# Kernel optimization log

Measured on AMD Instinct MI355X. Metric: run time of the kernel, lower is better.

Reference implementation:

```python
import jax, jax.numpy as jnp
import numpy as np

H = 2048          # hidden_size
I = 768           # moe_intermediate_size
E = 64            # num_experts
TOP_K = 8         # num_experts_per_tok (norm_topk_prob=True)
B, S = 1, 1024


def setup_inputs() -> dict:
    key = jax.random.key(0)
    ks = jax.random.split(key, 5)
    scale = 0.02
    return {
        "hidden_states": jax.random.normal(ks[0], (B, S, H), dtype=jnp.float32),
        "W_router": jax.random.normal(ks[1], (H, E), dtype=jnp.float32) * scale,
        "W_gate": jax.random.normal(ks[2], (E, H, I), dtype=jnp.float32) * scale,
        "W_up": jax.random.normal(ks[3], (E, H, I), dtype=jnp.float32) * scale,
        "W_down": jax.random.normal(ks[4], (E, I, H), dtype=jnp.float32) * scale,
    }


def reference(hidden_states, W_router, W_gate, W_up, W_down):
    b, s, h = hidden_states.shape
    x = hidden_states.reshape(-1, h)                      # [T, H]

    # --- Qwen3MoeTopKRouter: linear gate -> fp32 softmax -> top-k -> renorm ---
    logits = x @ W_router                                 # [T, E]
    probs = jax.nn.softmax(logits.astype(jnp.float32), axis=-1)
    top_w, top_idx = jax.lax.top_k(probs, TOP_K)          # [T, K]
    top_w = top_w / jnp.sum(top_w, axis=-1, keepdims=True)  # norm_topk_prob
    top_w = top_w.astype(x.dtype)

    # combine weights per (token, expert): zero if expert not selected
    comb = jnp.sum(jax.nn.one_hot(top_idx, E, dtype=x.dtype) * top_w[..., None], axis=1)  # [T, E]

    # --- per-expert SwiGLU MLP: down(silu(gate(x)) * up(x)), dense-masked ---
    g = jnp.einsum('th,ehi->eti', x, W_gate)              # [E, T, I]
    u = jnp.einsum('th,ehi->eti', x, W_up)                # [E, T, I]
    hmid = jax.nn.silu(g) * u                             # [E, T, I]
    # fold combine weight into the intermediate to avoid an [E, T, H] buffer
    hmid = hmid * comb.T[:, :, None]                      # [E, T, I]
    out = jnp.einsum('eti,eih->th', hmid, W_down)         # [T, H]

    return out.reshape(b, s, h)
```

## Files before the change

kernel.cpp:

```cpp
#include <hip/hip_runtime.h>
#include <hip/hip_bf16.h>

#define H_DIM 2048
#define I_DIM 768
#define NEXP 64
#define TOPK 8
#define NTOK 1024
#define BM 256
#define BKS 32

typedef float f32x4 __attribute__((ext_vector_type(4)));
typedef unsigned int u32x4 __attribute__((ext_vector_type(4)));
typedef unsigned int u32x2 __attribute__((ext_vector_type(2)));
typedef short bf16v8 __attribute__((ext_vector_type(8)));
typedef unsigned short u16x8 __attribute__((ext_vector_type(8)));
typedef unsigned int u32;

#define NTLOAD __builtin_nontemporal_load

#define WS_NEEDED 50954752ull

__device__ inline unsigned short f2bf(float f) {
    union { float f; u32 u; } v; v.f = f;
    u32 r = (v.u + 0x7FFFu + ((v.u >> 16) & 1u)) >> 16;
    return (unsigned short)r;
}
__device__ inline u32 pack2(float a, float b) {
    return (u32)f2bf(a) | ((u32)f2bf(b) << 16);
}

__device__ inline void async16(void* l, const void* g) {
    __builtin_amdgcn_global_load_lds(
        (const __attribute__((address_space(1))) unsigned int*)g,
        (__attribute__((address_space(3))) unsigned int*)l, 16, 0, 0);
}

__global__ void zero_kernel(float4* p, int n4) {
    int i = blockIdx.x * blockDim.x + threadIdx.x;
    if (i < n4) p[i] = (float4){0.f, 0.f, 0.f, 0.f};
}

__global__ __launch_bounds__(512) void router_kernel(
    const float* __restrict__ x, const float* __restrict__ Wr,
    int* __restrict__ topk_idx, float* __restrict__ topk_w,
    ushort4* __restrict__ xbf)
{
    const int t   = blockIdx.x;
    const int tid = threadIdx.x;
    const int lane = tid & 63;
    const int wv   = tid >> 6;
    __shared__ float xs[H_DIM];
    __shared__ float red[8][64];

    const float* xrow = x + (size_t)t * H_DIM;
    {
        const float4* src = (const float4*)xrow;
        float4 v = src[tid];
        ((float4*)xs)[tid] = v;
        ushort4 o;
        o.x = f2bf(v.x); o.y = f2bf(v.y); o.z = f2bf(v.z); o.w = f2bf(v.w);
        xbf[(size_t)t * (H_DIM / 4) + tid] = o;
    }
    __syncthreads();

    float acc = 0.f;
    const int h0 = wv * 256;
    #pragma unroll 8
    for (int h = h0; h < h0 + 256; ++h) acc += xs[h] * Wr[(size_t)h * NEXP + lane];
    red[wv][lane] = acc;
    __syncthreads();

    if (tid < 64) {
        const int e = tid;
        float logit = ((red[0][e] + red[1][e]) + (red[2][e] + red[3][e]))
                    + ((red[4][e] + red[5][e]) + (red[6][e] + red[7][e]));

        float m = logit;
        #pragma unroll
        for (int o = 32; o > 0; o >>= 1) m = fmaxf(m, __shfl_xor(m, o));
        float p = __expf(logit - m);
        float s = p;
        #pragma unroll
        for (int o = 32; o > 0; o >>= 1) s += __shfl_xor(s, o);
        float prob = p / s;

        float myp = prob;
        float kw[TOPK]; int kid[TOPK]; float wsum = 0.f;
        #pragma unroll
        for (int k = 0; k < TOPK; ++k) {
            float v = myp; int bi = e;
            #pragma unroll
            for (int o = 32; o > 0; o >>= 1) {
                float ov = __shfl_xor(v, o);
                int   oi = __shfl_xor(bi, o);
                if (ov > v || (ov == v && oi < bi)) { v = ov; bi = oi; }
            }
            kw[k] = v; kid[k] = bi; wsum += v;
            if (e == bi) myp = -1.f;
        }
        if (e == 0) {
            float inv = 1.f / wsum;
            #pragma unroll
            for (int k = 0; k < TOPK; ++k) {
                topk_idx[t * TOPK + k] = kid[k];
                topk_w[t * TOPK + k]   = kw[k] * inv;
            }
        }
    }
}

__global__ __launch_bounds__(64) void listbuild_kernel(
    const int* __restrict__ topk_idx, const float* __restrict__ topk_w,
    int* __restrict__ counts, int* __restrict__ lists, float* __restrict__ wlist,
    int* __restrict__ invmap)
{
    const int e = blockIdx.x;
    const int lane = threadIdx.x;
    int n = 0;
    for (int base = 0; base < NTOK * TOPK; base += 64) {
        int s = base + lane;
        int idx = topk_idx[s];
        bool match = (idx == e);
        unsigned long long mask = __ballot(match);
        int pre = __popcll(mask & ((1ull << lane) - 1ull));
        if (match) {
            lists[e * NTOK + n + pre] = s >> 3;
            wlist[e * NTOK + n + pre] = topk_w[s];
            invmap[s] = n + pre;
        }
        n += __popcll(mask);
    }
    if (lane == 0) counts[e] = n;
}

__global__ __launch_bounds__(64) void scan_kernel(
    const int* __restrict__ counts, int* __restrict__ offsets)
{
    int e = threadIdx.x;
    int v = counts[e];
    int xacc = v;
    #pragma unroll
    for (int o = 1; o < 64; o <<= 1) {
        int y = __shfl_up(xacc, o);
        if (e >= o) xacc += y;
    }
    offsets[e] = xacc - v;
}

#define MFMA_BF16 __builtin_amdgcn_mfma_f32_16x16x32_bf16
#define LGKM0()  asm volatile("s_waitcnt lgkmcnt(0)" ::: "memory")
#define RAWBAR() __builtin_amdgcn_s_barrier()
#define VMCNT4() asm volatile("s_waitcnt vmcnt(4)" ::: "memory")
#define VMCNT0() asm volatile("s_waitcnt vmcnt(0)" ::: "memory")
#define FENCE()  asm volatile("" ::: "memory")

__global__ __launch_bounds__(512) void gateup_kernel(
    const unsigned short* __restrict__ xbf,
    const float* __restrict__ Wg, const float* __restrict__ Wu,
    const int* __restrict__ counts, const int* __restrict__ offsets,
    const int* __restrict__ lists, const float* __restrict__ wlist,
    unsigned short* __restrict__ hmid)
{
    const int b  = blockIdx.x;
    const int wg = (b & 7) * 192 + (b >> 3);
    const int itile = wg % 24;
    const int e     = wg / 24;

    const int count = counts[e];
    if (count == 0) return;
    const int off = offsets[e];
    const int i0 = itile * 32;

    __shared__ unsigned short Alds[2][BM][32];
    __shared__ u32 Bgl[2][32 * 20];
    __shared__ u32 Bul[2][32 * 20];

    const int tid  = threadIdx.x;
    const int lane = tid & 63;
    const int wid  = tid >> 6;
    const int wm   = wid >> 1, wn = wid & 1;
    const int kb   = lane >> 4;
    const int l15  = lane & 15;

    const int bnn  = tid & 31;
    const int bkq  = (tid >> 5) & 7;
    const int bmat = tid >> 8;
    const float* WB = (bmat ? Wu : Wg) + (size_t)e * H_DIM * I_DIM + i0 + bnn;
    const int key4w = 4 * ((bnn >> 3) & 3);
    const int bwoff = bnn * 20 + ((2 * bkq) ^ key4w);
    const int brn   = wn * 16 + l15;
    const int key4r = 4 * ((brn >> 3) & 3);

    const int c4  = lane & 3;
    const int r0  = wid * 32 + (lane >> 2);
    const int r1  = r0 + 16;
    const int awr0 = wid * 32;
    const int awr1 = wid * 32 + 16;
    const int aoff = (wm * 64 + l15) * 32 + ((kb ^ ((l15 >> 1) & 3)) * 8);

    for (int mstart = 0; mstart < count; mstart += BM) {
        int p0 = mstart + r0; if (p0 >= count) p0 = count - 1;
        int p1 = mstart + r1; if (p1 >= count) p1 = count - 1;
        const unsigned short* srcA0 = xbf + (size_t)lists[e * NTOK + p0] * H_DIM
                                      + (size_t)((c4 ^ ((r0 >> 1) & 3)) * 8);
        const unsigned short* srcA1 = xbf + (size_t)lists[e * NTOK + p1] * H_DIM
                                      + (size_t)((c4 ^ ((r1 >> 1) & 3)) * 8);
        const bool mact = (mstart + wm * 64) < count;

        f32x4 accg[4], accu[4];
        #pragma unroll
        for (int i = 0; i < 4; ++i) {
            accg[i] = (f32x4){0.f, 0.f, 0.f, 0.f};
            accu[i] = (f32x4){0.f, 0.f, 0.f, 0.f};
        }

        float bA0, bA1, bA2, bA3;
        float bB0, bB1, bB2, bB3;

#define GU_LOADB(R0,R1,R2,R3,h)                                                 \
        {                                                                       \
            R0 = NTLOAD(WB + (size_t)((h) + 4 * bkq)     * I_DIM);              \
            R1 = NTLOAD(WB + (size_t)((h) + 4 * bkq + 1) * I_DIM);              \
            R2 = NTLOAD(WB + (size_t)((h) + 4 * bkq + 2) * I_DIM);              \
            R3 = NTLOAD(WB + (size_t)((h) + 4 * bkq + 3) * I_DIM);              \
        }
#define GU_STOREB(BUF,R0,R1,R2,R3)                                              \
        {                                                                       \
            u32x2 w_; w_.x = pack2(R0, R1); w_.y = pack2(R2, R3);               \
            *(u32x2*)((bmat ? Bul[BUF] : Bgl[BUF]) + bwoff) = w_;               \
        }
#define GU_DMAA(BUF,h)                                                          \
        {                                                                       \
            async16((void*)&Alds[BUF][awr0][0], (const void*)(srcA0 + (h)));    \
            async16((void*)&Alds[BUF][awr1][0], (const void*)(srcA1 + (h)));    \
        }
#define GU_MFMA(BUF)                                                            \
        if (mact) {                                                             \
            const unsigned short* Ab_ = (const unsigned short*)Alds[BUF];       \
            bf16v8 af[4], bg, bu;                                               \
            _Pragma("unroll")                                                   \
            for (int mf = 0; mf < 4; ++mf)                                      \
                af[mf] = *(const bf16v8*)&Ab_[aoff + mf * 512];                 \
            bg = *(const bf16v8*)&Bgl[BUF][brn * 20 + ((4 * kb) ^ key4r)];      \
            bu = *(const bf16v8*)&Bul[BUF][brn * 20 + ((4 * kb) ^ key4r)];      \
            _Pragma("unroll")                                                   \
            for (int mf = 0; mf < 4; ++mf) {                                    \
                accg[mf] = MFMA_BF16(af[mf], bg, accg[mf], 0, 0, 0);            \
                accu[mf] = MFMA_BF16(af[mf], bu, accu[mf], 0, 0, 0);            \
            }                                                                   \
        }
#define GU_PHASE(BUF,OBUF,R0,R1,R2,R3,nhB,nhA,VM)                               \
        GU_STOREB(BUF, R0, R1, R2, R3);                                         \
        if ((nhB) < H_DIM) GU_LOADB(R0, R1, R2, R3, (nhB));                     \
        VM();                                                                   \
        LGKM0();                                                                \
        RAWBAR();                                                               \
        FENCE();                                                                \
        if ((nhA) < H_DIM) GU_DMAA(OBUF, (nhA));                                \
        FENCE();                                                                \
        __builtin_amdgcn_s_setprio(1);                                          \
        GU_MFMA(BUF);                                                           \
        __builtin_amdgcn_s_setprio(0);

        GU_LOADB(bA0, bA1, bA2, bA3, 0);
        GU_LOADB(bB0, bB1, bB2, bB3, BKS);
        GU_DMAA(0, 0);

        for (int hh = 0; hh < H_DIM - 2 * BKS; hh += 2 * BKS) {
            GU_PHASE(0, 1, bA0, bA1, bA2, bA3, hh + 2 * BKS, hh + BKS,     VMCNT4);
            GU_PHASE(1, 0, bB0, bB1, bB2, bB3, hh + 3 * BKS, hh + 2 * BKS, VMCNT4);
        }
        GU_PHASE(0, 1, bA0, bA1, bA2, bA3, H_DIM, H_DIM - BKS, VMCNT0);
        GU_PHASE(1, 0, bB0, bB1, bB2, bB3, H_DIM, H_DIM,       VMCNT0);
        __syncthreads();
#undef GU_LOADB
#undef GU_STOREB
#undef GU_DMAA
#undef GU_MFMA
#undef GU_PHASE

        if (mact) {
            #pragma unroll
            for (int mf = 0; mf < 4; ++mf)
                #pragma unroll
                for (int r = 0; r < 4; ++r) {
                    int pos = mstart + wm * 64 + mf * 16 + kb * 4 + r;
                    if (pos < count) {
                        float wgt = wlist[e * NTOK + pos];
                        float g = accg[mf][r], u = accu[mf][r];
                        float s = 1.f / (1.f + __expf(-g));
                        hmid[(size_t)(off + pos) * I_DIM + i0 + wn * 16 + l15] = f2bf(g * s * u * wgt);
                    }
                }
        }
    }
}

template <bool USE_PART>
__global__ __launch_bounds__(512) void down_kernel(
    const unsigned short* __restrict__ hmid, const float* __restrict__ Wd,
    const int* __restrict__ counts, const int* __restrict__ offsets,
    const int* __restrict__ lists, float* __restrict__ out,
    unsigned short* __restrict__ part)
{
    const int b  = blockIdx.x;
    const int wg = (b & 7) * 512 + (b >> 3);
    const int htile = wg % 64;
    const int e     = wg / 64;

    const int count = counts[e];
    if (count == 0) return;
    const int off = offsets[e];
    const int h0 = htile * 32;

    __shared__ unsigned short Alds[2][BM][32];
    __shared__ u32 Bdl[2][32 * 20];

    const int tid  = threadIdx.x;
    const int lane = tid & 63;
    const int wid  = tid >> 6;
    const int wm   = wid >> 1, wn = wid & 1;
    const int kb   = lane >> 4;
    const int l15  = lane & 15;

    const int bnn  = tid & 31;
    const int bkq  = (tid >> 5) & 7;
    const bool bact = tid < 256;
    const float* WB = Wd + (size_t)e * I_DIM * H_DIM + h0 + bnn;
    const int key4w = 4 * ((bnn >> 3) & 3);
    const int bwoff = bnn * 20 + ((2 * bkq) ^ key4w);
    const int brn   = wn * 16 + l15;
    const int key4r = 4 * ((brn >> 3) & 3);

    const int c4  = lane & 3;
    const int r0  = wid * 32 + (lane >> 2);
    const int r1  = r0 + 16;
    const int awr0 = wid * 32;
    const int awr1 = wid * 32 + 16;
    const int aoff = (wm * 64 + l15) * 32 + ((kb ^ ((l15 >> 1) & 3)) * 8);

    for (int mstart = 0; mstart < count; mstart += BM) {
        int p0 = mstart + r0; if (p0 >= count) p0 = count - 1;
        int p1 = mstart + r1; if (p1 >= count) p1 = count - 1;
        const unsigned short* srcA0 = hmid + (size_t)(off + p0) * I_DIM
                                      + (size_t)((c4 ^ ((r0 >> 1) & 3)) * 8);
        const unsigned short* srcA1 = hmid + (size_t)(off + p1) * I_DIM
                                      + (size_t)((c4 ^ ((r1 >> 1) & 3)) * 8);
        const bool mact = (mstart + wm * 64) < count;

        f32x4 acc[4];
        #pragma unroll
        for (int i = 0; i < 4; ++i) acc[i] = (f32x4){0.f, 0.f, 0.f, 0.f};

        float bA0, bA1, bA2, bA3;
        float bB0, bB1, bB2, bB3;

#define DN_LOADB(R0,R1,R2,R3,k)                                                 \
        if (bact) {                                                             \
            R0 = NTLOAD(WB + (size_t)((k) + 4 * bkq)     * H_DIM);              \
            R1 = NTLOAD(WB + (size_t)((k) + 4 * bkq + 1) * H_DIM);              \
            R2 = NTLOAD(WB + (size_t)((k) + 4 * bkq + 2) * H_DIM);              \
            R3 = NTLOAD(WB + (size_t)((k) + 4 * bkq + 3) * H_DIM);              \
        }
#define DN_STOREB(BUF,R0,R1,R2,R3)                                              \
        if (bact) {                                                             \
            u32x2 w_; w_.x = pack2(R0, R1); w_.y = pack2(R2, R3);               \
            *(u32x2*)(Bdl[BUF] + bwoff) = w_;                                   \
        }
#define DN_DMAA(BUF,k)                                                          \
        {                                                                       \
            async16((void*)&Alds[BUF][awr0][0], (const void*)(srcA0 + (k)));    \
            async16((void*)&Alds[BUF][awr1][0], (const void*)(srcA1 + (k)));    \
        }
#define DN_MFMA(BUF)                                                            \
        if (mact) {                                                             \
            const unsigned short* Ab_ = (const unsigned short*)Alds[BUF];       \
            bf16v8 af[4], bd;                                                   \
            _Pragma("unroll")                                                   \
            for (int mf = 0; mf < 4; ++mf)                                      \
                af[mf] = *(const bf16v8*)&Ab_[aoff + mf * 512];                 \
            bd = *(const bf16v8*)&Bdl[BUF][brn * 20 + ((4 * kb) ^ key4r)];      \
            _Pragma("unroll")                                                   \
            for (int mf = 0; mf < 4; ++mf)                                      \
                acc[mf] = MFMA_BF16(af[mf], bd, acc[mf], 0, 0, 0);              \
        }
#define DN_VMS()  { if (bact) { VMCNT4(); } else { VMCNT0(); } }
#define DN_VMT()  VMCNT0()
#define DN_PHASE(BUF,OBUF,R0,R1,R2,R3,nkB,nkA,VM)                               \
        DN_STOREB(BUF, R0, R1, R2, R3);                                         \
        if ((nkB) < I_DIM) DN_LOADB(R0, R1, R2, R3, (nkB));                     \
        VM();                                                                   \
        LGKM0();                                                                \
        RAWBAR();                                                               \
        FENCE();                                                                \
        if ((nkA) < I_DIM) DN_DMAA(OBUF, (nkA));                                \
        FENCE();                                                                \
        __builtin_amdgcn_s_setprio(1);                                          \
        DN_MFMA(BUF);                                                           \
        __builtin_amdgcn_s_setprio(0);

        DN_LOADB(bA0, bA1, bA2, bA3, 0);
        DN_LOADB(bB0, bB1, bB2, bB3, BKS);
        DN_DMAA(0, 0);

        for (int ii = 0; ii < I_DIM - 2 * BKS; ii += 2 * BKS) {
            DN_PHASE(0, 1, bA0, bA1, bA2, bA3, ii + 2 * BKS, ii + BKS,     DN_VMS);
            DN_PHASE(1, 0, bB0, bB1, bB2, bB3, ii + 3 * BKS, ii + 2 * BKS, DN_VMS);
        }
        DN_PHASE(0, 1, bA0, bA1, bA2, bA3, I_DIM, I_DIM - BKS, DN_VMT);
        DN_PHASE(1, 0, bB0, bB1, bB2, bB3, I_DIM, I_DIM,       DN_VMT);
        __syncthreads();
#undef DN_LOADB
#undef DN_STOREB
#undef DN_DMAA
#undef DN_MFMA
#undef DN_VMS
#undef DN_VMT
#undef DN_PHASE

        if (mact) {
            #pragma unroll
            for (int mf = 0; mf < 4; ++mf)
                #pragma unroll
                for (int r = 0; r < 4; ++r) {
                    int pos = mstart + wm * 64 + mf * 16 + kb * 4 + r;
                    if (pos < count) {
                        if constexpr (USE_PART) {
                            part[(size_t)(off + pos) * H_DIM + h0 + wn * 16 + l15] =
                                f2bf(acc[mf][r]);
                        } else {
                            int tok = lists[e * NTOK + pos];
                            atomicAdd(&out[(size_t)tok * H_DIM + h0 + wn * 16 + l15],
                                      acc[mf][r]);
                        }
                    }
                }
        }
    }
}

__global__ __launch_bounds__(256) void reduce_kernel(
    const unsigned short* __restrict__ part,
    const int* __restrict__ topk_idx, const int* __restrict__ invmap,
    const int* __restrict__ offsets, float* __restrict__ out)
{
    const int t   = blockIdx.x;
    const int tid = threadIdx.x;
    __shared__ int slots[TOPK];
    if (tid < TOPK) {
        int s = t * TOPK + tid;
        slots[tid] = offsets[topk_idx[s]] + invmap[s];
    }
    __syncthreads();

    const int c = tid * 8;
    float acc[8] = {0.f, 0.f, 0.f, 0.f, 0.f, 0.f, 0.f, 0.f};
    #pragma unroll
    for (int k = 0; k < TOPK; ++k) {
        u16x8 v = *(const u16x8*)&part[(size_t)slots[k] * H_DIM + c];
        #pragma unroll
        for (int j = 0; j < 8; ++j)
            acc[j] += __uint_as_float((u32)(unsigned short)v[j] << 16);
    }
    float4* dst = (float4*)&out[(size_t)t * H_DIM + c];
    dst[0] = (float4){acc[0], acc[1], acc[2], acc[3]};
    dst[1] = (float4){acc[4], acc[5], acc[6], acc[7]};
}

extern "C" void kernel_launch(void* const* d_in, const int* in_sizes, int n_in,
                              void* d_out, int out_size, void* d_ws, size_t ws_size,
                              hipStream_t stream) {
    const float* x  = (const float*)d_in[0];
    const float* Wr = (const float*)d_in[1];
    const float* Wg = (const float*)d_in[2];
    const float* Wu = (const float*)d_in[3];
    const float* Wd = (const float*)d_in[4];
    float* out = (float*)d_out;

    char* ws = (char*)d_ws;
    int*   topk_idx = (int*)  (ws + 0);
    float* topk_w   = (float*)(ws + 32768);
    int*   counts   = (int*)  (ws + 65536);
    int*   offsets  = (int*)  (ws + 65792);
    int*   lists    = (int*)  (ws + 66048);
    float* wlist    = (float*)(ws + 328192);
    int*   invmap   = (int*)  (ws + 590336);
    unsigned short* hmid = (unsigned short*)(ws + 623104);
    unsigned short* xbf  = (unsigned short*)(ws + 13206016);
    unsigned short* part = (unsigned short*)(ws + 17400320);

    const bool usePart = ws_size >= WS_NEEDED;

    hipLaunchKernelGGL(router_kernel, dim3(NTOK), dim3(512), 0, stream,
                       x, Wr, topk_idx, topk_w, (ushort4*)xbf);
    hipLaunchKernelGGL(listbuild_kernel, dim3(NEXP), dim3(64), 0, stream,
                       topk_idx, topk_w, counts, lists, wlist, invmap);
    hipLaunchKernelGGL(scan_kernel, dim3(1), dim3(64), 0, stream,
                       counts, offsets);
    hipLaunchKernelGGL(gateup_kernel, dim3(24 * NEXP), dim3(512), 0, stream,
                       xbf, Wg, Wu, counts, offsets, lists, wlist, hmid);
    if (usePart) {
        hipLaunchKernelGGL((down_kernel<true>), dim3(64 * NEXP), dim3(512), 0, stream,
                           hmid, Wd, counts, offsets, lists, out, part);
        hipLaunchKernelGGL(reduce_kernel, dim3(NTOK), dim3(256), 0, stream,
                           part, topk_idx, invmap, offsets, out);
    } else {
        const int nout4 = NTOK * H_DIM / 4;
        hipLaunchKernelGGL(zero_kernel, dim3((nout4 + 255) / 256), dim3(256), 0, stream,
                           (float4*)out, nout4);
        hipLaunchKernelGGL((down_kernel<false>), dim3(64 * NEXP), dim3(512), 0, stream,
                           hmid, Wd, counts, offsets, lists, out, part);
    }
}
```

Before: 479.2 us.

## Widen N tile to 64 columns in gate/up and down expert GEMMs

```diff
diff --git a/kernel.cpp b/kernel.cpp
--- a/kernel.cpp
+++ b/kernel.cpp
@@ -148,11 +148,11 @@
 }
 
 #define MFMA_BF16 __builtin_amdgcn_mfma_f32_16x16x32_bf16
-#define LGKM0()  asm volatile("s_waitcnt lgkmcnt(0)" ::: "memory")
-#define RAWBAR() __builtin_amdgcn_s_barrier()
-#define VMCNT4() asm volatile("s_waitcnt vmcnt(4)" ::: "memory")
-#define VMCNT0() asm volatile("s_waitcnt vmcnt(0)" ::: "memory")
-#define FENCE()  asm volatile("" ::: "memory")
+#define LGKM0()   asm volatile("s_waitcnt lgkmcnt(0)" ::: "memory")
+#define RAWBAR()  __builtin_amdgcn_s_barrier()
+#define VMCNT8()  asm volatile("s_waitcnt vmcnt(8)" ::: "memory")
+#define VMCNT0()  asm volatile("s_waitcnt vmcnt(0)" ::: "memory")
+#define FENCE()   asm volatile("" ::: "memory")
 
 __global__ __launch_bounds__(512) void gateup_kernel(
     const unsigned short* __restrict__ xbf,
@@ -162,18 +162,18 @@
     unsigned short* __restrict__ hmid)
 {
     const int b  = blockIdx.x;
-    const int wg = (b & 7) * 192 + (b >> 3);
-    const int itile = wg % 24;
-    const int e     = wg / 24;
+    const int wg = (b & 7) * 96 + (b >> 3);
+    const int itile = wg % 12;
+    const int e     = wg / 12;
 
     const int count = counts[e];
     if (count == 0) return;
     const int off = offsets[e];
-    const int i0 = itile * 32;
+    const int i0 = itile * 64;
 
     __shared__ unsigned short Alds[2][BM][32];
-    __shared__ u32 Bgl[2][32 * 20];
-    __shared__ u32 Bul[2][32 * 20];
+    __shared__ u32 Bgl[2][64 * 20];
+    __shared__ u32 Bul[2][64 * 20];
 
     const int tid  = threadIdx.x;
     const int lane = tid & 63;
@@ -182,14 +182,16 @@
     const int kb   = lane >> 4;
     const int l15  = lane & 15;
 
-    const int bnn  = tid & 31;
-    const int bkq  = (tid >> 5) & 7;
+    const int bnn  = tid & 63;
+    const int bkq  = (tid >> 6) & 3;
     const int bmat = tid >> 8;
     const float* WB = (bmat ? Wu : Wg) + (size_t)e * H_DIM * I_DIM + i0 + bnn;
     const int key4w = 4 * ((bnn >> 3) & 3);
-    const int bwoff = bnn * 20 + ((2 * bkq) ^ key4w);
-    const int brn   = wn * 16 + l15;
-    const int key4r = 4 * ((brn >> 3) & 3);
+    const int bwoff = bnn * 20 + ((4 * bkq) ^ key4w);
+    const int brn0 = wn * 32 + l15;
+    const int brn1 = wn * 32 + 16 + l15;
+    const int key0 = 4 * ((brn0 >> 3) & 3);
+    const int key1 = 4 * ((brn1 >> 3) & 3);
 
     const int c4  = lane & 3;
     const int r0  = wid * 32 + (lane >> 2);
@@ -207,27 +209,32 @@
                                       + (size_t)((c4 ^ ((r1 >> 1) & 3)) * 8);
         const bool mact = (mstart + wm * 64) < count;
 
-        f32x4 accg[4], accu[4];
+        f32x4 accg[4][2], accu[4][2];
         #pragma unroll
-        for (int i = 0; i < 4; ++i) {
-            accg[i] = (f32x4){0.f, 0.f, 0.f, 0.f};
-            accu[i] = (f32x4){0.f, 0.f, 0.f, 0.f};
-        }
-
-        float bA0, bA1, bA2, bA3;
-        float bB0, bB1, bB2, bB3;
-
-#define GU_LOADB(R0,R1,R2,R3,h)                                                 \
+        for (int i = 0; i < 4; ++i)
+            #pragma unroll
+            for (int j = 0; j < 2; ++j) {
+                accg[i][j] = (f32x4){0.f, 0.f, 0.f, 0.f};
+                accu[i][j] = (f32x4){0.f, 0.f, 0.f, 0.f};
+            }
+
+        float sA0, sA1, sA2, sA3, sA4, sA5, sA6, sA7;
+        float sB0, sB1, sB2, sB3, sB4, sB5, sB6, sB7;
+
+#define GU_LOADB(S0,S1,S2,S3,S4,S5,S6,S7,h)                                     \
         {                                                                       \
-            R0 = NTLOAD(WB + (size_t)((h) + 4 * bkq)     * I_DIM);              \
-            R1 = NTLOAD(WB + (size_t)((h) + 4 * bkq + 1) * I_DIM);              \
-            R2 = NTLOAD(WB + (size_t)((h) + 4 * bkq + 2) * I_DIM);              \
-            R3 = NTLOAD(WB + (size_t)((h) + 4 * bkq + 3) * I_DIM);              \
-        }
-#define GU_STOREB(BUF,R0,R1,R2,R3)                                              \
+            const float* p_ = WB + (size_t)((h) + 8 * bkq) * I_DIM;             \
+            S0 = NTLOAD(p_);             S1 = NTLOAD(p_ + I_DIM);               \
+            S2 = NTLOAD(p_ + 2 * I_DIM); S3 = NTLOAD(p_ + 3 * I_DIM);           \
+            S4 = NTLOAD(p_ + 4 * I_DIM); S5 = NTLOAD(p_ + 5 * I_DIM);           \
+            S6 = NTLOAD(p_ + 6 * I_DIM); S7 = NTLOAD(p_ + 7 * I_DIM);           \
+        }
+#define GU_STOREB(BUF,S0,S1,S2,S3,S4,S5,S6,S7)                                  \
         {                                                                       \
-            u32x2 w_; w_.x = pack2(R0, R1); w_.y = pack2(R2, R3);               \
-            *(u32x2*)((bmat ? Bul[BUF] : Bgl[BUF]) + bwoff) = w_;               \
+            u32x4 w_;                                                           \
+            w_.x = pack2(S0, S1); w_.y = pack2(S2, S3);                         \
+            w_.z = pack2(S4, S5); w_.w = pack2(S6, S7);                         \
+            *(u32x4*)((bmat ? Bul[BUF] : Bgl[BUF]) + bwoff) = w_;               \
         }
 #define GU_DMAA(BUF,h)                                                          \
         {                                                                       \
@@ -237,41 +244,50 @@
 #define GU_MFMA(BUF)                                                            \
         if (mact) {                                                             \
             const unsigned short* Ab_ = (const unsigned short*)Alds[BUF];       \
-            bf16v8 af[4], bg, bu;                                               \
+            bf16v8 af[4];                                                       \
             _Pragma("unroll")                                                   \
             for (int mf = 0; mf < 4; ++mf)                                      \
                 af[mf] = *(const bf16v8*)&Ab_[aoff + mf * 512];                 \
-            bg = *(const bf16v8*)&Bgl[BUF][brn * 20 + ((4 * kb) ^ key4r)];      \
-            bu = *(const bf16v8*)&Bul[BUF][brn * 20 + ((4 * kb) ^ key4r)];      \
+            bf16v8 bg0 = *(const bf16v8*)&Bgl[BUF][brn0 * 20 + ((4 * kb) ^ key0)]; \
+            bf16v8 bg1 = *(const bf16v8*)&Bgl[BUF][brn1 * 20 + ((4 * kb) ^ key1)]; \
+            bf16v8 bu0 = *(const bf16v8*)&Bul[BUF][brn0 * 20 + ((4 * kb) ^ key0)]; \
+            bf16v8 bu1 = *(const bf16v8*)&Bul[BUF][brn1 * 20 + ((4 * kb) ^ key1)]; \
             _Pragma("unroll")                                                   \
             for (int mf = 0; mf < 4; ++mf) {                                    \
-                accg[mf] = MFMA_BF16(af[mf], bg, accg[mf], 0, 0, 0);            \
-                accu[mf] = MFMA_BF16(af[mf], bu, accu[mf], 0, 0, 0);            \
+                accg[mf][0] = MFMA_BF16(af[mf], bg0, accg[mf][0], 0, 0, 0);     \
+                accg[mf][1] = MFMA_BF16(af[mf], bg1, accg[mf][1], 0, 0, 0);     \
+                accu[mf][0] = MFMA_BF16(af[mf], bu0, accu[mf][0], 0, 0, 0);     \
+                accu[mf][1] = MFMA_BF16(af[mf], bu1, accu[mf][1], 0, 0, 0);     \
             }                                                                   \
         }
-#define GU_PHASE(BUF,OBUF,R0,R1,R2,R3,nhB,nhA,VM)                               \
-        GU_STOREB(BUF, R0, R1, R2, R3);                                         \
-        if ((nhB) < H_DIM) GU_LOADB(R0, R1, R2, R3, (nhB));                     \
+#define GU_PHASE(PB,S0,S1,S2,S3,S4,S5,S6,S7,nhB,nhA,VM)                         \
+        GU_STOREB(PB, S0, S1, S2, S3, S4, S5, S6, S7);                          \
+        if ((nhB) < H_DIM) GU_LOADB(S0, S1, S2, S3, S4, S5, S6, S7, (nhB));     \
         VM();                                                                   \
         LGKM0();                                                                \
         RAWBAR();                                                               \
         FENCE();                                                                \
-        if ((nhA) < H_DIM) GU_DMAA(OBUF, (nhA));                                \
+        if ((nhA) < H_DIM) GU_DMAA(PB ^ 1, (nhA));                              \
         FENCE();                                                                \
         __builtin_amdgcn_s_setprio(1);                                          \
-        GU_MFMA(BUF);                                                           \
+        GU_MFMA(PB);                                                            \
         __builtin_amdgcn_s_setprio(0);
 
-        GU_LOADB(bA0, bA1, bA2, bA3, 0);
-        GU_LOADB(bB0, bB1, bB2, bB3, BKS);
         GU_DMAA(0, 0);
-
-        for (int hh = 0; hh < H_DIM - 2 * BKS; hh += 2 * BKS) {
-            GU_PHASE(0, 1, bA0, bA1, bA2, bA3, hh + 2 * BKS, hh + BKS,     VMCNT4);
-            GU_PHASE(1, 0, bB0, bB1, bB2, bB3, hh + 3 * BKS, hh + 2 * BKS, VMCNT4);
-        }
-        GU_PHASE(0, 1, bA0, bA1, bA2, bA3, H_DIM, H_DIM - BKS, VMCNT0);
-        GU_PHASE(1, 0, bB0, bB1, bB2, bB3, H_DIM, H_DIM,       VMCNT0);
+        GU_LOADB(sA0, sA1, sA2, sA3, sA4, sA5, sA6, sA7, 0);
+        GU_LOADB(sB0, sB1, sB2, sB3, sB4, sB5, sB6, sB7, BKS);
+
+        for (int t2 = 0; t2 < 31; ++t2) {
+            const int hh = t2 * 2 * BKS;
+            GU_PHASE(0, sA0, sA1, sA2, sA3, sA4, sA5, sA6, sA7,
+                     hh + 2 * BKS, hh + BKS,     VMCNT8);
+            GU_PHASE(1, sB0, sB1, sB2, sB3, sB4, sB5, sB6, sB7,
+                     hh + 3 * BKS, hh + 2 * BKS, VMCNT8);
+        }
+        GU_PHASE(0, sA0, sA1, sA2, sA3, sA4, sA5, sA6, sA7,
+                 H_DIM, 63 * BKS, VMCNT0);
+        GU_PHASE(1, sB0, sB1, sB2, sB3, sB4, sB5, sB6, sB7,
+                 H_DIM, H_DIM,    VMCNT0);
         __syncthreads();
 #undef GU_LOADB
 #undef GU_STOREB
@@ -283,15 +299,18 @@
             #pragma unroll
             for (int mf = 0; mf < 4; ++mf)
                 #pragma unroll
-                for (int r = 0; r < 4; ++r) {
-                    int pos = mstart + wm * 64 + mf * 16 + kb * 4 + r;
-                    if (pos < count) {
-                        float wgt = wlist[e * NTOK + pos];
-                        float g = accg[mf][r], u = accu[mf][r];
-                        float s = 1.f / (1.f + __expf(-g));
-                        hmid[(size_t)(off + pos) * I_DIM + i0 + wn * 16 + l15] = f2bf(g * s * u * wgt);
+                for (int nf = 0; nf < 2; ++nf)
+                    #pragma unroll
+                    for (int r = 0; r < 4; ++r) {
+                        int pos = mstart + wm * 64 + mf * 16 + kb * 4 + r;
+                        if (pos < count) {
+                            float wgt = wlist[e * NTOK + pos];
+                            float g = accg[mf][nf][r], u = accu[mf][nf][r];
+                            float s = 1.f / (1.f + __expf(-g));
+                            hmid[(size_t)(off + pos) * I_DIM + i0 + wn * 32 + nf * 16 + l15]
+                                = f2bf(g * s * u * wgt);
+                        }
                     }
-                }
         }
     }
 }
@@ -304,17 +323,17 @@
     unsigned short* __restrict__ part)
 {
     const int b  = blockIdx.x;
-    const int wg = (b & 7) * 512 + (b >> 3);
-    const int htile = wg % 64;
-    const int e     = wg / 64;
+    const int wg = (b & 7) * 256 + (b >> 3);
+    const int htile = wg % 32;
+    const int e     = wg / 32;
 
     const int count = counts[e];
     if (count == 0) return;
     const int off = offsets[e];
-    const int h0 = htile * 32;
+    const int h0 = htile * 64;
 
     __shared__ unsigned short Alds[2][BM][32];
-    __shared__ u32 Bdl[2][32 * 20];
+    __shared__ u32 Bdl[2][64 * 20];
 
     const int tid  = threadIdx.x;
     const int lane = tid & 63;
@@ -323,14 +342,16 @@
     const int kb   = lane >> 4;
     const int l15  = lane & 15;
 
-    const int bnn  = tid & 31;
-    const int bkq  = (tid >> 5) & 7;
+    const int bnn  = tid & 63;
+    const int bkq  = (tid >> 6) & 3;
     const bool bact = tid < 256;
     const float* WB = Wd + (size_t)e * I_DIM * H_DIM + h0 + bnn;
     const int key4w = 4 * ((bnn >> 3) & 3);
-    const int bwoff = bnn * 20 + ((2 * bkq) ^ key4w);
-    const int brn   = wn * 16 + l15;
-    const int key4r = 4 * ((brn >> 3) & 3);
+    const int bwoff = bnn * 20 + ((4 * bkq) ^ key4w);
+    const int brn0 = wn * 32 + l15;
+    const int brn1 = wn * 32 + 16 + l15;
+    const int key0 = 4 * ((brn0 >> 3) & 3);
+    const int key1 = 4 * ((brn1 >> 3) & 3);
 
     const int c4  = lane & 3;
     const int r0  = wid * 32 + (lane >> 2);
@@ -348,24 +369,29 @@
                                       + (size_t)((c4 ^ ((r1 >> 1) & 3)) * 8);
         const bool mact = (mstart + wm * 64) < count;
 
-        f32x4 acc[4];
+        f32x4 acc[4][2];
         #pragma unroll
-        for (int i = 0; i < 4; ++i) acc[i] = (f32x4){0.f, 0.f, 0.f, 0.f};
-
-        float bA0, bA1, bA2, bA3;
-        float bB0, bB1, bB2, bB3;
-
-#define DN_LOADB(R0,R1,R2,R3,k)                                                 \
+        for (int i = 0; i < 4; ++i)
+            #pragma unroll
+            for (int j = 0; j < 2; ++j) acc[i][j] = (f32x4){0.f, 0.f, 0.f, 0.f};
+
+        float sA0, sA1, sA2, sA3, sA4, sA5, sA6, sA7;
+        float sB0, sB1, sB2, sB3, sB4, sB5, sB6, sB7;
+
+#define DN_LOADB(S0,S1,S2,S3,S4,S5,S6,S7,k)                                     \
         if (bact) {                                                             \
-            R0 = NTLOAD(WB + (size_t)((k) + 4 * bkq)     * H_DIM);              \
-            R1 = NTLOAD(WB + (size_t)((k) + 4 * bkq + 1) * H_DIM);              \
-            R2 = NTLOAD(WB + (size_t)((k) + 4 * bkq + 2) * H_DIM);              \
-            R3 = NTLOAD(WB + (size_t)((k) + 4 * bkq + 3) * H_DIM);              \
-        }
-#define DN_STOREB(BUF,R0,R1,R2,R3)                                              \
+            const float* p_ = WB + (size_t)((k) + 8 * bkq) * H_DIM;             \
+            S0 = NTLOAD(p_);             S1 = NTLOAD(p_ + H_DIM);               \
+            S2 = NTLOAD(p_ + 2 * H_DIM); S3 = NTLOAD(p_ + 3 * H_DIM);           \
+            S4 = NTLOAD(p_ + 4 * H_DIM); S5 = NTLOAD(p_ + 5 * H_DIM);           \
+            S6 = NTLOAD(p_ + 6 * H_DIM); S7 = NTLOAD(p_ + 7 * H_DIM);           \
+        }
+#define DN_STOREB(BUF,S0,S1,S2,S3,S4,S5,S6,S7)                                  \
         if (bact) {                                                             \
-            u32x2 w_; w_.x = pack2(R0, R1); w_.y = pack2(R2, R3);               \
-            *(u32x2*)(Bdl[BUF] + bwoff) = w_;                                   \
+            u32x4 w_;                                                           \
+            w_.x = pack2(S0, S1); w_.y = pack2(S2, S3);                         \
+            w_.z = pack2(S4, S5); w_.w = pack2(S6, S7);                         \
+            *(u32x4*)(Bdl[BUF] + bwoff) = w_;                                   \
         }
 #define DN_DMAA(BUF,k)                                                          \
         {                                                                       \
@@ -375,66 +401,74 @@
 #define DN_MFMA(BUF)                                                            \
         if (mact) {                                                             \
             const unsigned short* Ab_ = (const unsigned short*)Alds[BUF];       \
-            bf16v8 af[4], bd;                                                   \
+            bf16v8 af[4];                                                       \
             _Pragma("unroll")                                                   \
             for (int mf = 0; mf < 4; ++mf)                                      \
                 af[mf] = *(const bf16v8*)&Ab_[aoff + mf * 512];                 \
-            bd = *(const bf16v8*)&Bdl[BUF][brn * 20 + ((4 * kb) ^ key4r)];      \
+            bf16v8 bd0 = *(const bf16v8*)&Bdl[BUF][brn0 * 20 + ((4 * kb) ^ key0)]; \
+            bf16v8 bd1 = *(const bf16v8*)&Bdl[BUF][brn1 * 20 + ((4 * kb) ^ key1)]; \
             _Pragma("unroll")                                                   \
-            for (int mf = 0; mf < 4; ++mf)                                      \
-                acc[mf] = MFMA_BF16(af[mf], bd, acc[mf], 0, 0, 0);              \
-        }
-#define DN_VMS()  { if (bact) { VMCNT4(); } else { VMCNT0(); } }
-#define DN_VMT()  VMCNT0()
-#define DN_PHASE(BUF,OBUF,R0,R1,R2,R3,nkB,nkA,VM)                               \
-        DN_STOREB(BUF, R0, R1, R2, R3);                                         \
-        if ((nkB) < I_DIM) DN_LOADB(R0, R1, R2, R3, (nkB));                     \
+            for (int mf = 0; mf < 4; ++mf) {                                    \
+                acc[mf][0] = MFMA_BF16(af[mf], bd0, acc[mf][0], 0, 0, 0);       \
+                acc[mf][1] = MFMA_BF16(af[mf], bd1, acc[mf][1], 0, 0, 0);       \
+            }                                                                   \
+        }
+#define DN_VMS()  { if (bact) { VMCNT8(); } else { VMCNT0(); } }
+#define DN_PHASE(PB,S0,S1,S2,S3,S4,S5,S6,S7,nkB,nkA,VM)                         \
+        DN_STOREB(PB, S0, S1, S2, S3, S4, S5, S6, S7);                          \
+        if ((nkB) < I_DIM) DN_LOADB(S0, S1, S2, S3, S4, S5, S6, S7, (nkB));     \
         VM();                                                                   \
         LGKM0();                                                                \
         RAWBAR();                                                               \
         FENCE();                                                                \
-        if ((nkA) < I_DIM) DN_DMAA(OBUF, (nkA));                                \
+        if ((nkA) < I_DIM) DN_DMAA(PB ^ 1, (nkA));                              \
         FENCE();                                                                \
         __builtin_amdgcn_s_setprio(1);                                          \
-        DN_MFMA(BUF);                                                           \
+        DN_MFMA(PB);                                                            \
         __builtin_amdgcn_s_setprio(0);
 
-        DN_LOADB(bA0, bA1, bA2, bA3, 0);
-        DN_LOADB(bB0, bB1, bB2, bB3, BKS);
         DN_DMAA(0, 0);
-
-        for (int ii = 0; ii < I_DIM - 2 * BKS; ii += 2 * BKS) {
-            DN_PHASE(0, 1, bA0, bA1, bA2, bA3, ii + 2 * BKS, ii + BKS,     DN_VMS);
-            DN_PHASE(1, 0, bB0, bB1, bB2, bB3, ii + 3 * BKS, ii + 2 * BKS, DN_VMS);
-        }
-        DN_PHASE(0, 1, bA0, bA1, bA2, bA3, I_DIM, I_DIM - BKS, DN_VMT);
-        DN_PHASE(1, 0, bB0, bB1, bB2, bB3, I_DIM, I_DIM,       DN_VMT);
+        DN_LOADB(sA0, sA1, sA2, sA3, sA4, sA5, sA6, sA7, 0);
+        DN_LOADB(sB0, sB1, sB2, sB3, sB4, sB5, sB6, sB7, BKS);
+
+        for (int t2 = 0; t2 < 11; ++t2) {
+            const int ii = t2 * 2 * BKS;
+            DN_PHASE(0, sA0, sA1, sA2, sA3, sA4, sA5, sA6, sA7,
+                     ii + 2 * BKS, ii + BKS,     DN_VMS);
+            DN_PHASE(1, sB0, sB1, sB2, sB3, sB4, sB5, sB6, sB7,
+                     ii + 3 * BKS, ii + 2 * BKS, DN_VMS);
+        }
+        DN_PHASE(0, sA0, sA1, sA2, sA3, sA4, sA5, sA6, sA7,
+                 I_DIM, 23 * BKS, VMCNT0);
+        DN_PHASE(1, sB0, sB1, sB2, sB3, sB4, sB5, sB6, sB7,
+                 I_DIM, I_DIM,    VMCNT0);
         __syncthreads();
 #undef DN_LOADB
 #undef DN_STOREB
 #undef DN_DMAA
 #undef DN_MFMA
 #undef DN_VMS
-#undef DN_VMT
 #undef DN_PHASE
 
         if (mact) {
             #pragma unroll
             for (int mf = 0; mf < 4; ++mf)
                 #pragma unroll
-                for (int r = 0; r < 4; ++r) {
-                    int pos = mstart + wm * 64 + mf * 16 + kb * 4 + r;
-                    if (pos < count) {
-                        if constexpr (USE_PART) {
-                            part[(size_t)(off + pos) * H_DIM + h0 + wn * 16 + l15] =
-                                f2bf(acc[mf][r]);
-                        } else {
-                            int tok = lists[e * NTOK + pos];
-                            atomicAdd(&out[(size_t)tok * H_DIM + h0 + wn * 16 + l15],
-                                      acc[mf][r]);
+                for (int nf = 0; nf < 2; ++nf)
+                    #pragma unroll
+                    for (int r = 0; r < 4; ++r) {
+                        int pos = mstart + wm * 64 + mf * 16 + kb * 4 + r;
+                        if (pos < count) {
+                            if constexpr (USE_PART) {
+                                part[(size_t)(off + pos) * H_DIM + h0 + wn * 32 + nf * 16 + l15]
+                                    = f2bf(acc[mf][nf][r]);
+                            } else {
+                                int tok = lists[e * NTOK + pos];
+                                atomicAdd(&out[(size_t)tok * H_DIM + h0 + wn * 32 + nf * 16 + l15],
+                                          acc[mf][nf][r]);
+                            }
                         }
                     }
-                }
         }
     }
 }
@@ -497,10 +531,10 @@
                        topk_idx, topk_w, counts, lists, wlist, invmap);
     hipLaunchKernelGGL(scan_kernel, dim3(1), dim3(64), 0, stream,
                        counts, offsets);
-    hipLaunchKernelGGL(gateup_kernel, dim3(24 * NEXP), dim3(512), 0, stream,
+    hipLaunchKernelGGL(gateup_kernel, dim3(12 * NEXP), dim3(512), 0, stream,
                        xbf, Wg, Wu, counts, offsets, lists, wlist, hmid);
     if (usePart) {
-        hipLaunchKernelGGL((down_kernel<true>), dim3(64 * NEXP), dim3(512), 0, stream,
+        hipLaunchKernelGGL((down_kernel<true>), dim3(32 * NEXP), dim3(512), 0, stream,
                            hmid, Wd, counts, offsets, lists, out, part);
         hipLaunchKernelGGL(reduce_kernel, dim3(NTOK), dim3(256), 0, stream,
                            part, topk_idx, invmap, offsets, out);
@@ -508,7 +542,7 @@
         const int nout4 = NTOK * H_DIM / 4;
         hipLaunchKernelGGL(zero_kernel, dim3((nout4 + 255) / 256), dim3(256), 0, stream,
                            (float4*)out, nout4);
-        hipLaunchKernelGGL((down_kernel<false>), dim3(64 * NEXP), dim3(512), 0, stream,
+        hipLaunchKernelGGL((down_kernel<false>), dim3(32 * NEXP), dim3(512), 0, stream,
                            hmid, Wd, counts, offsets, lists, out, part);
     }
 }
```

New measurement: 486.8 us. Within noise of the previous version (+1.6%).
